# Kernel tuning notes

Hardware: AMD Instinct MI355X
Metric: run time of the kernel (lower is better)

Reference implementation:

```python
import jax, jax.numpy as jnp
import numpy as np
import math

V, P, D, L, H = 50257, 1024, 768, 12, 12
HD = D // H
DFF = 4 * D
B, S = 2, 1024
EPS = 1e-5


def setup_inputs() -> dict:
    key = jax.random.key(0)
    ks = jax.random.split(key, 8)
    sc = 0.02
    return {
        "input_ids": jax.random.randint(ks[0], (B, S), 0, V),
        "wte": jax.random.normal(ks[1], (V, D), jnp.float32) * sc,
        "wpe": jax.random.normal(ks[2], (P, D), jnp.float32) * sc,
        "ln1_g": jnp.ones((L, D), jnp.float32),
        "ln1_b": jnp.zeros((L, D), jnp.float32),
        "qkv_w": jax.random.normal(ks[3], (L, 3 * D, D), jnp.float32) * sc,
        "qkv_b": jnp.zeros((L, 3 * D), jnp.float32),
        "proj_w": jax.random.normal(ks[4], (L, D, D), jnp.float32) * sc,
        "proj_b": jnp.zeros((L, D), jnp.float32),
        "ln2_g": jnp.ones((L, D), jnp.float32),
        "ln2_b": jnp.zeros((L, D), jnp.float32),
        "fc_w": jax.random.normal(ks[5], (L, DFF, D), jnp.float32) * sc,
        "fc_b": jnp.zeros((L, DFF), jnp.float32),
        "cproj_w": jax.random.normal(ks[6], (L, D, DFF), jnp.float32) * sc,
        "cproj_b": jnp.zeros((L, D), jnp.float32),
        "lnf_g": jnp.ones((D,), jnp.float32),
        "lnf_b": jnp.zeros((D,), jnp.float32),
    }


def layer_norm(x, g, b):
    mu = jnp.mean(x, axis=-1, keepdims=True)
    var = jnp.mean(jnp.square(x - mu), axis=-1, keepdims=True)
    return (x - mu) * jax.lax.rsqrt(var + EPS) * g + b


def _forward(input_ids, wte, wpe, ln1_g, ln1_b, qkv_w, qkv_b, proj_w, proj_b,
             ln2_g, ln2_b, fc_w, fc_b, cproj_w, cproj_b, lnf_g, lnf_b):
    s = input_ids.shape[1]
    h = wte[input_ids] + wpe[jnp.arange(s)][None, :, :]  # [B,S,D]
    causal = jnp.tril(jnp.ones((s, s), bool))  # [S,S]
    neg_inf = jnp.finfo(h.dtype).min

    def step(x, p):
        l1g, l1b, qw, qb, pw, pb, l2g, l2b, fw, fb, cw, cb = p
        hn = layer_norm(x, l1g, l1b)
        qkv = hn @ qw.T + qb  # [B,S,3D]
        q, k, v = jnp.split(qkv, 3, axis=-1)
        q = q.reshape(B, s, H, HD).transpose(0, 2, 1, 3)  # [B,H,S,hd]
        k = k.reshape(B, s, H, HD).transpose(0, 2, 1, 3)
        v = v.reshape(B, s, H, HD).transpose(0, 2, 1, 3)
        scores = jnp.einsum("bhqd,bhkd->bhqk", q, k) / math.sqrt(HD)
        scores = jnp.where(causal[None, None], scores, neg_inf)
        attn = jax.nn.softmax(scores, axis=-1)
        o = jnp.einsum("bhqk,bhkd->bhqd", attn, v)
        o = o.transpose(0, 2, 1, 3).reshape(B, s, D)
        x = x + (o @ pw.T + pb)
        hn2 = layer_norm(x, l2g, l2b)
        m = jax.nn.gelu(hn2 @ fw.T + fb, approximate=False)
        x = x + (m @ cw.T + cb)
        return x, None

    params = (ln1_g, ln1_b, qkv_w, qkv_b, proj_w, proj_b,
              ln2_g, ln2_b, fc_w, fc_b, cproj_w, cproj_b)
    h, _ = jax.lax.scan(step, h, params)
    h = layer_norm(h, lnf_g, lnf_b)
    logits = h @ wte.T  # tied lm_head, [B,S,V]
    return logits


def reference(input_ids, wte, wpe, ln1_g, ln1_b, qkv_w, qkv_b, proj_w, proj_b,
              ln2_g, ln2_b, fc_w, fc_b, cproj_w, cproj_b, lnf_g, lnf_b):
    return _forward(input_ids, wte, wpe, ln1_g, ln1_b, qkv_w, qkv_b, proj_w,
                    proj_b, ln2_g, ln2_b, fc_w, fc_b, cproj_w, cproj_b,
                    lnf_g, lnf_b)
```

## Files before the change

kernel.cpp:

```cpp
#include <hip/hip_runtime.h>

#define BB 2
#define SS 1024
#define DM 768
#define NH 12
#define HDIM 64
#define NL 12
#define DFFN 3072
#define VOC 50257
#define ROWS (BB * SS)
#define MT (ROWS / 128)

typedef __attribute__((ext_vector_type(4))) float f32x4;
typedef __attribute__((ext_vector_type(8))) short short8;
typedef __attribute__((ext_vector_type(4))) short short4v;
typedef unsigned short ushort;

__device__ __forceinline__ ushort f2bf(float f) {
  union { float f; unsigned int u; } x; x.f = f;
  unsigned int u = x.u;
  unsigned int r = (u + 0x7FFFu + ((u >> 16) & 1u)) >> 16;
  return (ushort)r;
}

__global__ __launch_bounds__(256) void embed_k(const int* __restrict__ ids,
    const float* __restrict__ wte, const float* __restrict__ wpe,
    float* __restrict__ h) {
  const int row = blockIdx.x;
  const int s = row & (SS - 1);
  const int tid = threadIdx.x;
  const int id = ids[row];
  const size_t wbase = (size_t)id * DM;
  const size_t pbase = (size_t)s * DM;
  const size_t obase = (size_t)row * DM;
  h[obase + tid]       = wte[wbase + tid]       + wpe[pbase + tid];
  h[obase + tid + 256] = wte[wbase + tid + 256] + wpe[pbase + tid + 256];
  h[obase + tid + 512] = wte[wbase + tid + 512] + wpe[pbase + tid + 512];
}

__global__ __launch_bounds__(256) void f2b_k(const float* __restrict__ in,
                                             ushort* __restrict__ out, int n4) {
  for (int i = blockIdx.x * 256 + threadIdx.x; i < n4; i += gridDim.x * 256) {
    f32x4 v = ((const f32x4*)in)[i];
    short4v s;
    s[0] = f2bf(v[0]); s[1] = f2bf(v[1]); s[2] = f2bf(v[2]); s[3] = f2bf(v[3]);
    ((short4v*)out)[i] = s;
  }
}

template <int OB>
__global__ __launch_bounds__(256) void layernorm_t(const float* __restrict__ x,
    const float* __restrict__ g, const float* __restrict__ b, void* __restrict__ y) {
  const int tid = threadIdx.x;
  const size_t base = (size_t)blockIdx.x * DM;
  float v0 = x[base + tid], v1 = x[base + tid + 256], v2 = x[base + tid + 512];
  __shared__ float red[256];
  red[tid] = v0 + v1 + v2;
  __syncthreads();
  for (int off = 128; off > 0; off >>= 1) {
    if (tid < off) red[tid] += red[tid + off];
    __syncthreads();
  }
  float mu = red[0] * (1.0f / DM);
  __syncthreads();
  float d0 = v0 - mu, d1 = v1 - mu, d2 = v2 - mu;
  red[tid] = d0 * d0 + d1 * d1 + d2 * d2;
  __syncthreads();
  for (int off = 128; off > 0; off >>= 1) {
    if (tid < off) red[tid] += red[tid + off];
    __syncthreads();
  }
  float rstd = rsqrtf(red[0] * (1.0f / DM) + 1e-5f);
  float o0 = d0 * rstd * g[tid]       + b[tid];
  float o1 = d1 * rstd * g[tid + 256] + b[tid + 256];
  float o2 = d2 * rstd * g[tid + 512] + b[tid + 512];
  if (OB) {
    ushort* yo = (ushort*)y;
    yo[base + tid] = f2bf(o0); yo[base + tid + 256] = f2bf(o1);
    yo[base + tid + 512] = f2bf(o2);
  } else {
    float* yo = (float*)y;
    yo[base + tid] = o0; yo[base + tid + 256] = o1; yo[base + tid + 512] = o2;
  }
}

template <int ROUNDS>
__device__ __forceinline__ void stage_sw(const ushort* __restrict__ g, int ldg,
                                         ushort* lds, int wave, int lane,
                                         int rowmax) {
#pragma unroll
  for (int r = 0; r < ROUNDS; r++) {
    const int chunk = (r * 4 + wave) * 64 + lane;
    const int nrow = chunk >> 3;
    const int cs = (chunk & 7) ^ (nrow & 7);
    const int row = nrow > rowmax ? rowmax : nrow;
    const ushort* ga = g + (size_t)row * ldg + cs * 8;
    ushort* la = lds + (r * 4 + wave) * 512;
    __builtin_amdgcn_global_load_lds(
        (const __attribute__((address_space(1))) unsigned int*)ga,
        (__attribute__((address_space(3))) unsigned int*)la, 16, 0, 0);
  }
}

template <int EPI, int OUTBF, int NF>
__global__ __launch_bounds__(256) void gemm_bf(const ushort* __restrict__ A,
    const ushort* __restrict__ Bw, const float* __restrict__ bias,
    const float* __restrict__ res, void* __restrict__ Cout, int N, int K) {
  __shared__ __align__(16) ushort AsL[2][128 * 64];
  __shared__ __align__(16) ushort BsL[2][NF * 32 * 64];
  const int tid = threadIdx.x;
  const int lane = tid & 63;
  const int wave = tid >> 6;
  const int la = lane & 15;
  const int hi = lane >> 4;
  const int swz = (la & 7) << 3;

  const int nwg = gridDim.x;
  int bid = blockIdx.x;
  {
    const int q = nwg >> 3, r = nwg & 7;
    const int xcd = bid & 7, idx = bid >> 3;
    bid = (xcd < r ? xcd * (q + 1) : r * (q + 1) + (xcd - r) * q) + idx;
  }
  const int m0 = (bid % MT) * 128;
  const int n0 = (bid / MT) * (NF * 32);

  const int wr = (wave >> 1) * 64;
  const int wc = (wave & 1) * (NF * 16);
  const int brmax = min(N - n0 - 1, NF * 32 - 1);

  f32x4 acc[4][NF];
#pragma unroll
  for (int i = 0; i < 4; i++)
#pragma unroll
    for (int j = 0; j < NF; j++) acc[i][j] = (f32x4){0.f, 0.f, 0.f, 0.f};

  const ushort* Ag = A + (size_t)m0 * K;
  const ushort* Bg = Bw + (size_t)n0 * K;

  const int nt = K >> 6;
  const int s0 = (bid % MT) % nt;

  stage_sw<4>(Ag + s0 * 64, K, AsL[0], wave, lane, 127);
  stage_sw<NF>(Bg + s0 * 64, K, BsL[0], wave, lane, brmax);

  int cur = 0;
  for (int t = 0; t < nt; t++) {
    if (t + 1 < nt) {
      int sn = t + 1 + s0; if (sn >= nt) sn -= nt;
      stage_sw<4>(Ag + sn * 64, K, AsL[cur ^ 1], wave, lane, 127);
      stage_sw<NF>(Bg + sn * 64, K, BsL[cur ^ 1], wave, lane, brmax);
      asm volatile("s_waitcnt vmcnt(%0)" :: "i"(4 + NF) : "memory");
    } else {
      asm volatile("s_waitcnt vmcnt(0)" ::: "memory");
    }
    __builtin_amdgcn_s_barrier();
    __builtin_amdgcn_sched_barrier(0);

    const ushort* Ab = AsL[cur] + (wr + la) * 64;
    const ushort* Bb = BsL[cur] + (wc + la) * 64;
    __builtin_amdgcn_s_setprio(1);
#pragma unroll
    for (int ks = 0; ks < 2; ks++) {
      const int co = (ks * 32 + hi * 8) ^ swz;
      short8 a[4], b[NF];
#pragma unroll
      for (int mi = 0; mi < 4; mi++)
        a[mi] = *(const short8*)(Ab + mi * 1024 + co);
#pragma unroll
      for (int ni = 0; ni < NF; ni++)
        b[ni] = *(const short8*)(Bb + ni * 1024 + co);
#pragma unroll
      for (int mi = 0; mi < 4; mi++)
#pragma unroll
        for (int ni = 0; ni < NF; ni++)
          acc[mi][ni] = __builtin_amdgcn_mfma_f32_16x16x32_bf16(
              a[mi], b[ni], acc[mi][ni], 0, 0, 0);
    }
    __builtin_amdgcn_s_setprio(0);
    __builtin_amdgcn_sched_barrier(0);
    __builtin_amdgcn_s_barrier();
    __builtin_amdgcn_sched_barrier(0);
    cur ^= 1;
  }

#pragma unroll
  for (int mi = 0; mi < 4; mi++)
#pragma unroll
    for (int ni = 0; ni < NF; ni++) {
      const int col = n0 + wc + ni * 16 + la;
      if (col < N) {
#pragma unroll
        for (int j = 0; j < 4; j++) {
          const int row = m0 + wr + mi * 16 + 4 * hi + j;
          float x = acc[mi][ni][j];
          if (EPI >= 1) x += bias[col];
          const size_t idx = (size_t)row * N + col;
          if (EPI == 2) x += res[idx];
          if (EPI == 3) x = 0.5f * x * (1.0f + erff(x * 0.70710678118f));
          if (OUTBF) ((ushort*)Cout)[idx] = f2bf(x);
          else       ((float*)Cout)[idx] = x;
        }
      }
    }
}

template <int EPI, int OUTBF, int MR>
__global__ __launch_bounds__(256) void gemm_p3(const ushort* __restrict__ A,
    const ushort* __restrict__ Bw, const float* __restrict__ bias,
    const float* __restrict__ res, void* __restrict__ Cout, int N, int K) {
  constexpr int MROWS = MR * 32;
  constexpr int MTILES = ROWS / MROWS;
  constexpr int ASZ = MROWS * 64;
  constexpr int BSZ = 64 * 64;
  __shared__ __align__(16) ushort smem[3 * ASZ + 3 * BSZ];
  ushort* As = smem;
  ushort* Bs = smem + 3 * ASZ;

  const int tid = threadIdx.x;
  const int lane = tid & 63;
  const int wave = tid >> 6;
  const int la = lane & 15;
  const int hi = lane >> 4;
  const int swz = (la & 7) << 3;

  const int nwg = gridDim.x;
  int bid = blockIdx.x;
  {
    const int q = nwg >> 3, r = nwg & 7;
    const int xcd = bid & 7, idx = bid >> 3;
    bid = (xcd < r ? xcd * (q + 1) : r * (q + 1) + (xcd - r) * q) + idx;
  }
  const int m0 = (bid % MTILES) * MROWS;
  const int n0 = (bid / MTILES) * 64;

  const int wr = (wave >> 1) * (MROWS / 2);
  const int wc = (wave & 1) * 32;

  f32x4 acc[MR][2];
#pragma unroll
  for (int i = 0; i < MR; i++)
#pragma unroll
    for (int j = 0; j < 2; j++) acc[i][j] = (f32x4){0.f, 0.f, 0.f, 0.f};

  const ushort* Ag = A + (size_t)m0 * K;
  const ushort* Bg = Bw + (size_t)n0 * K;
  const int nt = K >> 6;
  const int s0 = (bid % MTILES) % nt;

  {
    int s1 = s0 + 1; if (s1 >= nt) s1 -= nt;
    stage_sw<MR>(Ag + s0 * 64, K, As, wave, lane, MROWS - 1);
    stage_sw<2>(Bg + s0 * 64, K, Bs, wave, lane, 63);
    stage_sw<MR>(Ag + s1 * 64, K, As + ASZ, wave, lane, MROWS - 1);
    stage_sw<2>(Bg + s1 * 64, K, Bs + BSZ, wave, lane, 63);
  }

  for (int t = 0; t < nt; t++) {
    if (t + 1 < nt) {
      asm volatile("s_waitcnt vmcnt(%0)" :: "i"(MR + 2) : "memory");
    } else {
      asm volatile("s_waitcnt vmcnt(0)" ::: "memory");
    }
    __builtin_amdgcn_s_barrier();
    __builtin_amdgcn_sched_barrier(0);

    const ushort* Ab = As + (t % 3) * ASZ + (wr + la) * 64;
    const ushort* Bb = Bs + (t % 3) * BSZ + (wc + la) * 64;
    __builtin_amdgcn_s_setprio(1);
#pragma unroll
    for (int ks = 0; ks < 2; ks++) {
      const int co = (ks * 32 + hi * 8) ^ swz;
      short8 a[MR], b[2];
#pragma unroll
      for (int mi = 0; mi < MR; mi++)
        a[mi] = *(const short8*)(Ab + mi * 1024 + co);
#pragma unroll
      for (int ni = 0; ni < 2; ni++)
        b[ni] = *(const short8*)(Bb + ni * 1024 + co);
#pragma unroll
      for (int mi = 0; mi < MR; mi++)
#pragma unroll
        for (int ni = 0; ni < 2; ni++)
          acc[mi][ni] = __builtin_amdgcn_mfma_f32_16x16x32_bf16(
              a[mi], b[ni], acc[mi][ni], 0, 0, 0);
    }
    __builtin_amdgcn_s_setprio(0);
    __builtin_amdgcn_sched_barrier(0);
    __builtin_amdgcn_s_barrier();
    __builtin_amdgcn_sched_barrier(0);
    if (t + 2 < nt) {
      int sn = t + 2 + s0; if (sn >= nt) sn -= nt;
      stage_sw<MR>(Ag + sn * 64, K, As + ((t + 2) % 3) * ASZ, wave, lane, MROWS - 1);
      stage_sw<2>(Bg + sn * 64, K, Bs + ((t + 2) % 3) * BSZ, wave, lane, 63);
    }
  }

  if (OUTBF) {
    ushort* L = smem;
#pragma unroll
    for (int mi = 0; mi < MR; mi++)
#pragma unroll
      for (int ni = 0; ni < 2; ni++)
#pragma unroll
        for (int j = 0; j < 4; j++) {
          const int row = wr + mi * 16 + 4 * hi + j;
          const int col = wc + ni * 16 + la;
          float x = acc[mi][ni][j];
          if (EPI >= 1) x += bias[n0 + col];
          if (EPI == 3) x = 0.5f * x * (1.0f + erff(x * 0.70710678118f));
          L[row * 72 + col] = f2bf(x);
        }
    __syncthreads();
    ushort* Co = (ushort*)Cout;
    constexpr int ITERS = MROWS * 64 / 8 / 256;
#pragma unroll
    for (int it = 0; it < ITERS; it++) {
      const int idx8 = it * 256 + tid;
      const int row = idx8 >> 3, c8 = idx8 & 7;
      short8 v = *(const short8*)&L[row * 72 + c8 * 8];
      *(short8*)&Co[(size_t)(m0 + row) * N + n0 + c8 * 8] = v;
    }
  } else {
    float* L = (float*)smem;
#pragma unroll
    for (int mi = 0; mi < MR; mi++)
#pragma unroll
      for (int ni = 0; ni < 2; ni++)
#pragma unroll
        for (int j = 0; j < 4; j++) {
          const int row = wr + mi * 16 + 4 * hi + j;
          const int col = wc + ni * 16 + la;
          float x = acc[mi][ni][j];
          if (EPI >= 1) x += bias[n0 + col];
          if (EPI == 3) x = 0.5f * x * (1.0f + erff(x * 0.70710678118f));
          L[row * 68 + col] = x;
        }
    __syncthreads();
    f32x4* Co = (f32x4*)Cout;
    const f32x4* R4 = (const f32x4*)res;
    constexpr int ITERS = MROWS * 64 / 4 / 256;
#pragma unroll
    for (int it = 0; it < ITERS; it++) {
      const int idx4 = it * 256 + tid;
      const int row = idx4 >> 4, c4 = idx4 & 15;
      f32x4 v = *(const f32x4*)&L[row * 68 + c4 * 4];
      const size_t o4 = ((size_t)(m0 + row) * N + n0) / 4 + c4;
      if (EPI == 2) v += R4[o4];
      Co[o4] = v;
    }
  }
}

__global__ __launch_bounds__(256) void attn_bf(const ushort* __restrict__ qkv,
                                               ushort* __restrict__ o) {
  const int tid = threadIdx.x;
  const int lane = tid & 63;
  const int wave = tid >> 6;
  const int hi = lane >> 4;
  const int la = lane & 15;
  const int q0 = blockIdx.x * 64;
  const int bh = blockIdx.y;
  const int bb = bh / NH;
  const int hh = bh % NH;
  const size_t rstride = 3 * DM;
  const ushort* base = qkv + (size_t)bb * SS * rstride;

  __shared__ ushort Ks[64][72];
  __shared__ ushort Vt[64][72];
  __shared__ ushort Pb[4][16][72];

  short8 qf[2];
  {
    const int qrow = q0 + wave * 16 + la;
    const ushort* qp = base + (size_t)qrow * rstride + hh * HDIM + 8 * hi;
    qf[0] = *(const short8*)qp;
    qf[1] = *(const short8*)(qp + 32);
  }

  f32x4 accO[4] = {};
  float m_[4], l_[4];
#pragma unroll
  for (int j = 0; j < 4; j++) { m_[j] = -1e30f; l_[j] = 0.f; }

  const int nt = q0 / 64 + 1;
  for (int kt = 0; kt < nt; kt++) {
    __syncthreads();
    {
      const int r = tid >> 2;
      const int c = (tid & 3) * 16;
      const ushort* kp = base + (size_t)(kt * 64 + r) * rstride + DM + hh * HDIM + c;
      const ushort* vp = kp + DM;
      *(short8*)&Ks[r][c]     = *(const short8*)kp;
      *(short8*)&Ks[r][c + 8] = *(const short8*)(kp + 8);
      short8 v0 = *(const short8*)vp;
      short8 v1 = *(const short8*)(vp + 8);
#pragma unroll
      for (int i = 0; i < 8; i++) {
        Vt[c + i][r]     = (ushort)v0[i];
        Vt[c + 8 + i][r] = (ushort)v1[i];
      }
    }
    __syncthreads();

    f32x4 s[4] = {};
#pragma unroll
    for (int f = 0; f < 4; f++) {
#pragma unroll
      for (int kk = 0; kk < 2; kk++) {
        short8 kf = *(const short8*)&Ks[f * 16 + la][kk * 32 + 8 * hi];
        s[f] = __builtin_amdgcn_mfma_f32_16x16x32_bf16(qf[kk], kf, s[f], 0, 0, 0);
      }
#pragma unroll
      for (int j = 0; j < 4; j++) s[f][j] *= 0.125f;
    }

    if (kt == nt - 1) {
      const int qr = wave * 16 + 4 * hi;
#pragma unroll
      for (int f = 0; f < 4; f++) {
        const int kcol = f * 16 + la;
#pragma unroll
        for (int j = 0; j < 4; j++)
          if (kcol > qr + j) s[f][j] = -1e30f;
      }
    }

#pragma unroll
    for (int j = 0; j < 4; j++) {
      float rm = fmaxf(fmaxf(s[0][j], s[1][j]), fmaxf(s[2][j], s[3][j]));
      rm = fmaxf(rm, __shfl_xor(rm, 1));
      rm = fmaxf(rm, __shfl_xor(rm, 2));
      rm = fmaxf(rm, __shfl_xor(rm, 4));
      rm = fmaxf(rm, __shfl_xor(rm, 8));
      const float mnew = fmaxf(m_[j], rm);
      const float alpha = expf(m_[j] - mnew);
      float rs = 0.f;
#pragma unroll
      for (int f = 0; f < 4; f++) {
        const float p = expf(s[f][j] - mnew);
        s[f][j] = p;
        rs += p;
      }
      rs += __shfl_xor(rs, 1);
      rs += __shfl_xor(rs, 2);
      rs += __shfl_xor(rs, 4);
      rs += __shfl_xor(rs, 8);
      l_[j] = l_[j] * alpha + rs;
      m_[j] = mnew;
#pragma unroll
      for (int f = 0; f < 4; f++) accO[f][j] *= alpha;
    }

#pragma unroll
    for (int f = 0; f < 4; f++)
#pragma unroll
      for (int j = 0; j < 4; j++)
        Pb[wave][4 * hi + j][f * 16 + la] = f2bf(s[f][j]);

    short8 pf0 = *(const short8*)&Pb[wave][la][8 * hi];
    short8 pf1 = *(const short8*)&Pb[wave][la][32 + 8 * hi];
#pragma unroll
    for (int f = 0; f < 4; f++) {
      short8 vf0 = *(const short8*)&Vt[f * 16 + la][8 * hi];
      short8 vf1 = *(const short8*)&Vt[f * 16 + la][32 + 8 * hi];
      accO[f] = __builtin_amdgcn_mfma_f32_16x16x32_bf16(pf0, vf0, accO[f], 0, 0, 0);
      accO[f] = __builtin_amdgcn_mfma_f32_16x16x32_bf16(pf1, vf1, accO[f], 0, 0, 0);
    }
  }

  ushort* op = o + (size_t)(bb * SS + q0 + wave * 16) * DM + hh * HDIM;
#pragma unroll
  for (int j = 0; j < 4; j++) {
    const float inv = 1.0f / l_[j];
    const int qr = 4 * hi + j;
#pragma unroll
    for (int f = 0; f < 4; f++)
      op[(size_t)qr * DM + f * 16 + la] = f2bf(accO[f][j] * inv);
  }
}

template <int EPI>
__global__ __launch_bounds__(256) void gemm_nt(const float* __restrict__ A,
    const float* __restrict__ Bw, const float* __restrict__ bias,
    const float* __restrict__ res, float* __restrict__ C, int N, int K) {
  __shared__ ushort As[64][40];
  __shared__ ushort Bs[64][40];
  const int tid = threadIdx.x;
  const int m0 = blockIdx.y * 64;
  const int n0 = blockIdx.x * 64;
  const int lane = tid & 63;
  const int wave = tid >> 6;
  const int wr = (wave >> 1) * 32;
  const int wc = (wave & 1) * 32;
  const int lr = lane & 15;
  const int lk = (lane >> 4) * 8;
  const int sr = tid >> 2;
  const int sc = (tid & 3) * 8;
  f32x4 acc[2][2] = {};
  for (int kk = 0; kk < K; kk += 32) {
    {
      const float* p = A + (size_t)(m0 + sr) * K + kk + sc;
      f32x4 v0 = *(const f32x4*)p;
      f32x4 v1 = *(const f32x4*)(p + 4);
      short8 sv;
      for (int i = 0; i < 4; i++) { sv[i] = f2bf(v0[i]); sv[4 + i] = f2bf(v1[i]); }
      *(short8*)&As[sr][sc] = sv;
    }
    {
      const int gr = n0 + sr;
      short8 sv = {};
      if (gr < N) {
        const float* p = Bw + (size_t)gr * K + kk + sc;
        f32x4 v0 = *(const f32x4*)p;
        f32x4 v1 = *(const f32x4*)(p + 4);
        for (int i = 0; i < 4; i++) { sv[i] = f2bf(v0[i]); sv[4 + i] = f2bf(v1[i]); }
      }
      *(short8*)&Bs[sr][sc] = sv;
    }
    __syncthreads();
    short8 a0 = *(const short8*)&As[wr + lr][lk];
    short8 a1 = *(const short8*)&As[wr + 16 + lr][lk];
    short8 b0 = *(const short8*)&Bs[wc + lr][lk];
    short8 b1 = *(const short8*)&Bs[wc + 16 + lr][lk];
    acc[0][0] = __builtin_amdgcn_mfma_f32_16x16x32_bf16(a0, b0, acc[0][0], 0, 0, 0);
    acc[0][1] = __builtin_amdgcn_mfma_f32_16x16x32_bf16(a0, b1, acc[0][1], 0, 0, 0);
    acc[1][0] = __builtin_amdgcn_mfma_f32_16x16x32_bf16(a1, b0, acc[1][0], 0, 0, 0);
    acc[1][1] = __builtin_amdgcn_mfma_f32_16x16x32_bf16(a1, b1, acc[1][1], 0, 0, 0);
    __syncthreads();
  }
  const int orow = (lane >> 4) * 4;
  for (int mi = 0; mi < 2; mi++)
    for (int ni = 0; ni < 2; ni++) {
      const int col = n0 + wc + ni * 16 + lr;
      if (col >= N) continue;
      for (int j = 0; j < 4; j++) {
        const int row = m0 + wr + mi * 16 + orow + j;
        float x = acc[mi][ni][j];
        if (EPI >= 1) x += bias[col];
        const size_t idx = (size_t)row * N + col;
        if (EPI == 2) x += res[idx];
        if (EPI == 3) x = 0.5f * x * (1.0f + erff(x * 0.70710678118f));
        C[idx] = x;
      }
    }
}

__global__ __launch_bounds__(256) void attn_f32(const float* __restrict__ qkv,
                                                float* __restrict__ o) {
  const int tid = threadIdx.x;
  const int lane = tid & 63;
  const int wave = tid >> 6;
  const int hi = lane >> 4;
  const int la = lane & 15;
  const int q0 = blockIdx.x * 64;
  const int bh = blockIdx.y;
  const int bb = bh / NH;
  const int hh = bh % NH;
  const size_t rstride = 3 * DM;
  const float* base = qkv + (size_t)bb * SS * rstride;
  __shared__ ushort Ks[64][72];
  __shared__ ushort Vt[64][72];
  __shared__ ushort Pb[4][16][72];
  short8 qf[2];
  {
    const int qrow = q0 + wave * 16 + la;
    const float* qp = base + (size_t)qrow * rstride + hh * HDIM + 8 * hi;
    for (int kk = 0; kk < 2; kk++) {
      f32x4 v0 = *(const f32x4*)(qp + 32 * kk);
      f32x4 v1 = *(const f32x4*)(qp + 32 * kk + 4);
      short8 sv;
      for (int i = 0; i < 4; i++) {
        sv[i] = f2bf(v0[i] * 0.125f); sv[4 + i] = f2bf(v1[i] * 0.125f);
      }
      qf[kk] = sv;
    }
  }
  f32x4 accO[4] = {};
  float m_[4], l_[4];
  for (int j = 0; j < 4; j++) { m_[j] = -1e30f; l_[j] = 0.f; }
  const int nt = q0 / 64 + 1;
  for (int kt = 0; kt < nt; kt++) {
    __syncthreads();
    {
      const int r = tid >> 2;
      const int c = (tid & 3) * 16;
      const float* kp = base + (size_t)(kt * 64 + r) * rstride + DM + hh * HDIM + c;
      const float* vp = kp + DM;
      f32x4 k0 = *(const f32x4*)kp, k1 = *(const f32x4*)(kp + 4);
      f32x4 k2 = *(const f32x4*)(kp + 8), k3 = *(const f32x4*)(kp + 12);
      short8 s0, s1;
      for (int i = 0; i < 4; i++) {
        s0[i] = f2bf(k0[i]); s0[4 + i] = f2bf(k1[i]);
        s1[i] = f2bf(k2[i]); s1[4 + i] = f2bf(k3[i]);
      }
      *(short8*)&Ks[r][c] = s0;
      *(short8*)&Ks[r][c + 8] = s1;
      f32x4 v0 = *(const f32x4*)vp, v1 = *(const f32x4*)(vp + 4);
      f32x4 v2 = *(const f32x4*)(vp + 8), v3 = *(const f32x4*)(vp + 12);
      for (int i = 0; i < 4; i++) {
        Vt[c + i][r] = f2bf(v0[i]); Vt[c + 4 + i][r] = f2bf(v1[i]);
        Vt[c + 8 + i][r] = f2bf(v2[i]); Vt[c + 12 + i][r] = f2bf(v3[i]);
      }
    }
    __syncthreads();
    f32x4 s[4] = {};
    for (int f = 0; f < 4; f++)
      for (int kk = 0; kk < 2; kk++) {
        short8 kf = *(const short8*)&Ks[f * 16 + la][kk * 32 + 8 * hi];
        s[f] = __builtin_amdgcn_mfma_f32_16x16x32_bf16(qf[kk], kf, s[f], 0, 0, 0);
      }
    if (kt == nt - 1) {
      const int qr = wave * 16 + 4 * hi;
      for (int f = 0; f < 4; f++) {
        const int kcol = f * 16 + la;
        for (int j = 0; j < 4; j++)
          if (kcol > qr + j) s[f][j] = -1e30f;
      }
    }
    for (int j = 0; j < 4; j++) {
      float rm = fmaxf(fmaxf(s[0][j], s[1][j]), fmaxf(s[2][j], s[3][j]));
      rm = fmaxf(rm, __shfl_xor(rm, 1));
      rm = fmaxf(rm, __shfl_xor(rm, 2));
      rm = fmaxf(rm, __shfl_xor(rm, 4));
      rm = fmaxf(rm, __shfl_xor(rm, 8));
      const float mnew = fmaxf(m_[j], rm);
      const float alpha = expf(m_[j] - mnew);
      float rs = 0.f;
      for (int f = 0; f < 4; f++) {
        const float p = expf(s[f][j] - mnew);
        s[f][j] = p; rs += p;
      }
      rs += __shfl_xor(rs, 1);
      rs += __shfl_xor(rs, 2);
      rs += __shfl_xor(rs, 4);
      rs += __shfl_xor(rs, 8);
      l_[j] = l_[j] * alpha + rs;
      m_[j] = mnew;
      for (int f = 0; f < 4; f++) accO[f][j] *= alpha;
    }
    for (int f = 0; f < 4; f++)
      for (int j = 0; j < 4; j++)
        Pb[wave][4 * hi + j][f * 16 + la] = f2bf(s[f][j]);
    short8 pf0 = *(const short8*)&Pb[wave][la][8 * hi];
    short8 pf1 = *(const short8*)&Pb[wave][la][32 + 8 * hi];
    for (int f = 0; f < 4; f++) {
      short8 vf0 = *(const short8*)&Vt[f * 16 + la][8 * hi];
      short8 vf1 = *(const short8*)&Vt[f * 16 + la][32 + 8 * hi];
      accO[f] = __builtin_amdgcn_mfma_f32_16x16x32_bf16(pf0, vf0, accO[f], 0, 0, 0);
      accO[f] = __builtin_amdgcn_mfma_f32_16x16x32_bf16(pf1, vf1, accO[f], 0, 0, 0);
    }
  }
  float* op = o + (size_t)(bb * SS + q0 + wave * 16) * DM + hh * HDIM;
  for (int j = 0; j < 4; j++) {
    const float inv = 1.0f / l_[j];
    const int qr = 4 * hi + j;
    for (int f = 0; f < 4; f++)
      op[(size_t)qr * DM + f * 16 + la] = accO[f][j] * inv;
  }
}

extern "C" void kernel_launch(void* const* d_in, const int* in_sizes, int n_in,
                              void* d_out, int out_size, void* d_ws,
                              size_t ws_size, hipStream_t stream) {
  const int*   ids     = (const int*)d_in[0];
  const float* wte     = (const float*)d_in[1];
  const float* wpe     = (const float*)d_in[2];
  const float* ln1_g   = (const float*)d_in[3];
  const float* ln1_b   = (const float*)d_in[4];
  const float* qkv_w   = (const float*)d_in[5];
  const float* qkv_b   = (const float*)d_in[6];
  const float* proj_w  = (const float*)d_in[7];
  const float* proj_b  = (const float*)d_in[8];
  const float* ln2_g   = (const float*)d_in[9];
  const float* ln2_b   = (const float*)d_in[10];
  const float* fc_w    = (const float*)d_in[11];
  const float* fc_b    = (const float*)d_in[12];
  const float* cproj_w = (const float*)d_in[13];
  const float* cproj_b = (const float*)d_in[14];
  const float* lnf_g   = (const float*)d_in[15];
  const float* lnf_b   = (const float*)d_in[16];
  float* out = (float*)d_out;

  const size_t sz_h    = (size_t)ROWS * DM * 4;
  const size_t sz_hn   = (size_t)ROWS * DM * 2;
  const size_t sz_qkv  = (size_t)ROWS * 3 * DM * 2;
  const size_t sz_ob   = (size_t)ROWS * DM * 2;
  const size_t sz_mb   = (size_t)ROWS * DFFN * 2;
  const size_t sz_wq   = (size_t)NL * 3 * DM * DM * 2;
  const size_t sz_wp   = (size_t)NL * DM * DM * 2;
  const size_t sz_wf   = (size_t)NL * DFFN * DM * 2;
  const size_t sz_wc   = (size_t)NL * DM * DFFN * 2;
  const size_t sz_wt   = (size_t)VOC * DM * 2;
  const size_t NEED = sz_h + sz_hn + sz_qkv + sz_ob + sz_mb +
                      sz_wq + sz_wp + sz_wf + sz_wc + sz_wt;

  if (ws_size >= NEED) {
    char* p = (char*)d_ws;
    float*  h    = (float*)p;  p += sz_h;
    ushort* hn   = (ushort*)p; p += sz_hn;
    ushort* qkvb = (ushort*)p; p += sz_qkv;
    ushort* ob   = (ushort*)p; p += sz_ob;
    ushort* mb   = (ushort*)p; p += sz_mb;
    ushort* wq   = (ushort*)p; p += sz_wq;
    ushort* wp   = (ushort*)p; p += sz_wp;
    ushort* wf   = (ushort*)p; p += sz_wf;
    ushort* wc   = (ushort*)p; p += sz_wc;
    ushort* wt   = (ushort*)p; p += sz_wt;

    f2b_k<<<2048, 256, 0, stream>>>(qkv_w,   wq, NL * 3 * DM * DM / 4);
    f2b_k<<<1024, 256, 0, stream>>>(proj_w,  wp, NL * DM * DM / 4);
    f2b_k<<<2048, 256, 0, stream>>>(fc_w,    wf, NL * DFFN * DM / 4);
    f2b_k<<<2048, 256, 0, stream>>>(cproj_w, wc, NL * DM * DFFN / 4);
    f2b_k<<<2048, 256, 0, stream>>>(wte,     wt, VOC * DM / 4);

    embed_k<<<ROWS, 256, 0, stream>>>(ids, wte, wpe, h);

    for (int l = 0; l < NL; l++) {
      layernorm_t<1><<<ROWS, 256, 0, stream>>>(h, ln1_g + l * DM, ln1_b + l * DM, hn);
      gemm_p3<1, 1, 4><<<MT * (3 * DM / 64), 256, 0, stream>>>(
          hn, wq + (size_t)l * 3 * DM * DM, qkv_b + (size_t)l * 3 * DM,
          nullptr, qkvb, 3 * DM, DM);
      attn_bf<<<dim3(SS / 64, BB * NH), 256, 0, stream>>>(qkvb, ob);
      gemm_p3<2, 0, 2><<<(ROWS / 64) * (DM / 64), 256, 0, stream>>>(
          ob, wp + (size_t)l * DM * DM, proj_b + (size_t)l * DM, h, h, DM, DM);
      layernorm_t<1><<<ROWS, 256, 0, stream>>>(h, ln2_g + l * DM, ln2_b + l * DM, hn);
      gemm_p3<3, 1, 4><<<MT * (DFFN / 64), 256, 0, stream>>>(
          hn, wf + (size_t)l * DFFN * DM, fc_b + (size_t)l * DFFN,
          nullptr, mb, DFFN, DM);
      gemm_p3<2, 0, 2><<<(ROWS / 64) * (DM / 64), 256, 0, stream>>>(
          mb, wc + (size_t)l * DM * DFFN, cproj_b + (size_t)l * DM, h, h,
          DM, DFFN);
    }

    layernorm_t<1><<<ROWS, 256, 0, stream>>>(h, lnf_g, lnf_b, hn);
    gemm_bf<0, 0, 4><<<MT * ((VOC + 127) / 128), 256, 0, stream>>>(
        hn, wt, nullptr, nullptr, out, VOC, DM);
  } else {
    float* ws = (float*)d_ws;
    float* h   = ws;
    float* hn  = h + (size_t)ROWS * DM;
    float* qkv = hn + (size_t)ROWS * DM;
    float* ob  = qkv + (size_t)ROWS * 3 * DM;
    float* mb  = ob + (size_t)ROWS * DM;

    embed_k<<<ROWS, 256, 0, stream>>>(ids, wte, wpe, h);
    for (int l = 0; l < NL; l++) {
      layernorm_t<0><<<ROWS, 256, 0, stream>>>(h, ln1_g + l * DM, ln1_b + l * DM, hn);
      gemm_nt<1><<<dim3(3 * DM / 64, ROWS / 64), 256, 0, stream>>>(
          hn, qkv_w + (size_t)l * 3 * DM * DM, qkv_b + (size_t)l * 3 * DM,
          nullptr, qkv, 3 * DM, DM);
      attn_f32<<<dim3(SS / 64, BB * NH), 256, 0, stream>>>(qkv, ob);
      gemm_nt<2><<<dim3(DM / 64, ROWS / 64), 256, 0, stream>>>(
          ob, proj_w + (size_t)l * DM * DM, proj_b + (size_t)l * DM, h, h, DM, DM);
      layernorm_t<0><<<ROWS, 256, 0, stream>>>(h, ln2_g + l * DM, ln2_b + l * DM, hn);
      gemm_nt<3><<<dim3(DFFN / 64, ROWS / 64), 256, 0, stream>>>(
          hn, fc_w + (size_t)l * DFFN * DM, fc_b + (size_t)l * DFFN,
          nullptr, mb, DFFN, DM);
      gemm_nt<2><<<dim3(DM / 64, ROWS / 64), 256, 0, stream>>>(
          mb, cproj_w + (size_t)l * DM * DFFN, cproj_b + (size_t)l * DM, h, h,
          DM, DFFN);
    }
    layernorm_t<0><<<ROWS, 256, 0, stream>>>(h, lnf_g, lnf_b, hn);
    gemm_nt<0><<<dim3((VOC + 63) / 64, ROWS / 64), 256, 0, stream>>>(
        hn, wte, nullptr, nullptr, out, VOC, DM);
  }
}
```

Baseline: 2.073 ms.

## Stage LM-head GEMM output through LDS and prefetch attention K/V tiles

The LM-head GEMM is specialised into gemm_lg, which writes the accumulator tile to shared memory in two 64-column halves and then stores rows with coalesced fp32 writes. This targets the strided epilogue stores into the large logits array. Separately, the attention kernel now prefetches the next K/V tile into registers while the current one is being computed. The V transpose into LDS now packs two rows per 32-bit store instead of scattering single 16-bit writes. The cost is extra barriers in the GEMM epilogue and higher register pressure in attention.

```diff
diff --git a/kernel.cpp b/kernel.cpp
--- a/kernel.cpp
+++ b/kernel.cpp
@@ -102,12 +102,14 @@
   }
 }
 
-template <int EPI, int OUTBF, int NF>
-__global__ __launch_bounds__(256) void gemm_bf(const ushort* __restrict__ A,
-    const ushort* __restrict__ Bw, const float* __restrict__ bias,
-    const float* __restrict__ res, void* __restrict__ Cout, int N, int K) {
-  __shared__ __align__(16) ushort AsL[2][128 * 64];
-  __shared__ __align__(16) ushort BsL[2][NF * 32 * 64];
+__global__ __launch_bounds__(256) void gemm_lg(const ushort* __restrict__ A,
+    const ushort* __restrict__ Bw, float* __restrict__ Cout, int N, int K) {
+  __shared__ __align__(16) ushort smem[4 * 8192];
+  ushort* AsL0 = smem;
+  ushort* AsL1 = smem + 8192;
+  ushort* BsL0 = smem + 16384;
+  ushort* BsL1 = smem + 24576;
+
   const int tid = threadIdx.x;
   const int lane = tid & 63;
   const int wave = tid >> 6;
@@ -123,17 +125,17 @@
     bid = (xcd < r ? xcd * (q + 1) : r * (q + 1) + (xcd - r) * q) + idx;
   }
   const int m0 = (bid % MT) * 128;
-  const int n0 = (bid / MT) * (NF * 32);
+  const int n0 = (bid / MT) * 128;
 
   const int wr = (wave >> 1) * 64;
-  const int wc = (wave & 1) * (NF * 16);
-  const int brmax = min(N - n0 - 1, NF * 32 - 1);
-
-  f32x4 acc[4][NF];
+  const int wc = (wave & 1) * 64;
+  const int brmax = min(N - n0 - 1, 127);
+
+  f32x4 acc[4][4];
 #pragma unroll
   for (int i = 0; i < 4; i++)
 #pragma unroll
-    for (int j = 0; j < NF; j++) acc[i][j] = (f32x4){0.f, 0.f, 0.f, 0.f};
+    for (int j = 0; j < 4; j++) acc[i][j] = (f32x4){0.f, 0.f, 0.f, 0.f};
 
   const ushort* Ag = A + (size_t)m0 * K;
   const ushort* Bg = Bw + (size_t)n0 * K;
@@ -141,39 +143,39 @@
   const int nt = K >> 6;
   const int s0 = (bid % MT) % nt;
 
-  stage_sw<4>(Ag + s0 * 64, K, AsL[0], wave, lane, 127);
-  stage_sw<NF>(Bg + s0 * 64, K, BsL[0], wave, lane, brmax);
+  stage_sw<4>(Ag + s0 * 64, K, AsL0, wave, lane, 127);
+  stage_sw<4>(Bg + s0 * 64, K, BsL0, wave, lane, brmax);
 
   int cur = 0;
   for (int t = 0; t < nt; t++) {
     if (t + 1 < nt) {
       int sn = t + 1 + s0; if (sn >= nt) sn -= nt;
-      stage_sw<4>(Ag + sn * 64, K, AsL[cur ^ 1], wave, lane, 127);
-      stage_sw<NF>(Bg + sn * 64, K, BsL[cur ^ 1], wave, lane, brmax);
-      asm volatile("s_waitcnt vmcnt(%0)" :: "i"(4 + NF) : "memory");
+      stage_sw<4>(Ag + sn * 64, K, cur ? AsL0 : AsL1, wave, lane, 127);
+      stage_sw<4>(Bg + sn * 64, K, cur ? BsL0 : BsL1, wave, lane, brmax);
+      asm volatile("s_waitcnt vmcnt(8)" ::: "memory");
     } else {
       asm volatile("s_waitcnt vmcnt(0)" ::: "memory");
     }
     __builtin_amdgcn_s_barrier();
     __builtin_amdgcn_sched_barrier(0);
 
-    const ushort* Ab = AsL[cur] + (wr + la) * 64;
-    const ushort* Bb = BsL[cur] + (wc + la) * 64;
+    const ushort* Ab = (cur ? AsL1 : AsL0) + (wr + la) * 64;
+    const ushort* Bb = (cur ? BsL1 : BsL0) + (wc + la) * 64;
     __builtin_amdgcn_s_setprio(1);
 #pragma unroll
     for (int ks = 0; ks < 2; ks++) {
       const int co = (ks * 32 + hi * 8) ^ swz;
-      short8 a[4], b[NF];
+      short8 a[4], b[4];
 #pragma unroll
       for (int mi = 0; mi < 4; mi++)
         a[mi] = *(const short8*)(Ab + mi * 1024 + co);
 #pragma unroll
-      for (int ni = 0; ni < NF; ni++)
+      for (int ni = 0; ni < 4; ni++)
         b[ni] = *(const short8*)(Bb + ni * 1024 + co);
 #pragma unroll
       for (int mi = 0; mi < 4; mi++)
 #pragma unroll
-        for (int ni = 0; ni < NF; ni++)
+        for (int ni = 0; ni < 4; ni++)
           acc[mi][ni] = __builtin_amdgcn_mfma_f32_16x16x32_bf16(
               a[mi], b[ni], acc[mi][ni], 0, 0, 0);
     }
@@ -184,25 +186,33 @@
     cur ^= 1;
   }
 
-#pragma unroll
-  for (int mi = 0; mi < 4; mi++)
-#pragma unroll
-    for (int ni = 0; ni < NF; ni++) {
-      const int col = n0 + wc + ni * 16 + la;
-      if (col < N) {
-#pragma unroll
-        for (int j = 0; j < 4; j++) {
-          const int row = m0 + wr + mi * 16 + 4 * hi + j;
-          float x = acc[mi][ni][j];
-          if (EPI >= 1) x += bias[col];
-          const size_t idx = (size_t)row * N + col;
-          if (EPI == 2) x += res[idx];
-          if (EPI == 3) x = 0.5f * x * (1.0f + erff(x * 0.70710678118f));
-          if (OUTBF) ((ushort*)Cout)[idx] = f2bf(x);
-          else       ((float*)Cout)[idx] = x;
-        }
-      }
-    }
+  float* L = (float*)smem;
+  const int myhalf = wave & 1;
+#pragma unroll
+  for (int h = 0; h < 2; h++) {
+    if (myhalf == h) {
+#pragma unroll
+      for (int mi = 0; mi < 4; mi++)
+#pragma unroll
+        for (int ni = 0; ni < 4; ni++)
+#pragma unroll
+          for (int j = 0; j < 4; j++) {
+            const int row = wr + mi * 16 + 4 * hi + j;
+            const int col = ni * 16 + la;
+            L[row * 68 + col] = acc[mi][ni][j];
+          }
+    }
+    __syncthreads();
+#pragma unroll
+    for (int it = 0; it < 32; it++) {
+      const int flat = it * 256 + tid;
+      const int row = flat >> 6, col = flat & 63;
+      const int gc = n0 + h * 64 + col;
+      if (gc < N)
+        Cout[(size_t)(m0 + row) * N + gc] = L[row * 68 + col];
+    }
+    __syncthreads();
+  }
 }
 
 template <int EPI, int OUTBF, int MR>
@@ -365,10 +375,17 @@
   const int hh = bh % NH;
   const size_t rstride = 3 * DM;
   const ushort* base = qkv + (size_t)bb * SS * rstride;
+  const ushort* kbase = base + DM + hh * HDIM;
+  const ushort* vbase = base + 2 * DM + hh * HDIM;
 
   __shared__ ushort Ks[64][72];
   __shared__ ushort Vt[64][72];
   __shared__ ushort Pb[4][16][72];
+
+  const int kr = tid >> 2;
+  const int kc = (tid & 3) * 16;
+  const int vp0 = (tid >> 3) * 2;
+  const int vc = (tid & 7) * 8;
 
   short8 qf[2];
   {
@@ -378,6 +395,16 @@
     qf[1] = *(const short8*)(qp + 32);
   }
 
+  short8 kA, kB, vA, vB;
+  {
+    const ushort* kp = kbase + (size_t)kr * rstride + kc;
+    kA = *(const short8*)kp;
+    kB = *(const short8*)(kp + 8);
+    const ushort* vp = vbase + (size_t)vp0 * rstride + vc;
+    vA = *(const short8*)vp;
+    vB = *(const short8*)(vp + rstride);
+  }
+
   f32x4 accO[4] = {};
   float m_[4], l_[4];
 #pragma unroll
@@ -386,22 +413,23 @@
   const int nt = q0 / 64 + 1;
   for (int kt = 0; kt < nt; kt++) {
     __syncthreads();
-    {
-      const int r = tid >> 2;
-      const int c = (tid & 3) * 16;
-      const ushort* kp = base + (size_t)(kt * 64 + r) * rstride + DM + hh * HDIM + c;
-      const ushort* vp = kp + DM;
-      *(short8*)&Ks[r][c]     = *(const short8*)kp;
-      *(short8*)&Ks[r][c + 8] = *(const short8*)(kp + 8);
-      short8 v0 = *(const short8*)vp;
-      short8 v1 = *(const short8*)(vp + 8);
-#pragma unroll
-      for (int i = 0; i < 8; i++) {
-        Vt[c + i][r]     = (ushort)v0[i];
-        Vt[c + 8 + i][r] = (ushort)v1[i];
-      }
-    }
-    __syncthreads();
+    *(short8*)&Ks[kr][kc]     = kA;
+    *(short8*)&Ks[kr][kc + 8] = kB;
+#pragma unroll
+    for (int i = 0; i < 8; i++) {
+      unsigned int pk = (unsigned int)(unsigned short)vA[i] |
+                        ((unsigned int)(unsigned short)vB[i] << 16);
+      *(unsigned int*)&Vt[vc + i][vp0] = pk;
+    }
+    __syncthreads();
+    if (kt + 1 < nt) {
+      const ushort* kp = kbase + (size_t)((kt + 1) * 64 + kr) * rstride + kc;
+      kA = *(const short8*)kp;
+      kB = *(const short8*)(kp + 8);
+      const ushort* vp = vbase + (size_t)((kt + 1) * 64 + vp0) * rstride + vc;
+      vA = *(const short8*)vp;
+      vB = *(const short8*)(vp + rstride);
+    }
 
     f32x4 s[4] = {};
 #pragma unroll
@@ -734,8 +762,8 @@
     }
 
     layernorm_t<1><<<ROWS, 256, 0, stream>>>(h, lnf_g, lnf_b, hn);
-    gemm_bf<0, 0, 4><<<MT * ((VOC + 127) / 128), 256, 0, stream>>>(
-        hn, wt, nullptr, nullptr, out, VOC, DM);
+    gemm_lg<<<MT * ((VOC + 127) / 128), 256, 0, stream>>>(
+        hn, wt, out, VOC, DM);
   } else {
     float* ws = (float*)d_ws;
     float* h   = ws;
```

Result: no change. 2.036 ms (-1.8%).
